# Optimization experiments

Hardware: AMD Instinct MI355X
Metric: run time of the kernel (lower is better)

## Reference

```python
import jax, jax.numpy as jnp
import numpy as np
from jax import lax

B_, L, DM = 2, 2048, 1024
DI, N, K, R = 2048, 16, 4, 64  # d_inner, d_state, d_conv, dt_rank
EPS = 1e-5


def setup_inputs() -> dict:
    key = jax.random.key(0)
    ks = jax.random.split(key, 12)
    w = lambda k, s: (jax.random.normal(k, s, dtype=jnp.float32) * 0.02)
    inp = {
        "x": jax.random.normal(ks[0], (B_, L, DM), dtype=jnp.float32),
        "hormone_vectors": jax.random.normal(ks[1], (B_, 64), dtype=jnp.float32),
        "norm_w": jnp.ones((DM,), dtype=jnp.float32),
        "in_proj_w": w(ks[2], (DM, 2 * DI)),
        "conv_w": w(ks[3], (DI, K)),
        "conv_b": jnp.zeros((DI,), dtype=jnp.float32),
        "x_proj_w": w(ks[4], (DI, R + 2 * N)),
        "dt_proj_w": w(ks[5], (R, DI)),
        "dt_proj_b": jax.random.uniform(ks[6], (DI,), dtype=jnp.float32, minval=-4.0, maxval=-2.0),
        "A_log": jnp.log(jnp.broadcast_to(jnp.arange(1, N + 1, dtype=jnp.float32), (DI, N))),
        "D": jnp.ones((DI,), dtype=jnp.float32),
        "out_proj_w": w(ks[7], (DI, DM)),
    }
    return inp


def _rmsnorm(x, w, eps=EPS):
    var = jnp.mean(x * x, axis=-1, keepdims=True)
    return x * lax.rsqrt(var + eps) * w


def _causal_depthwise_conv(u, conv_w, conv_b):
    # u: [B,L,DI] -> causal depthwise conv along L with kernel K
    lhs = jnp.transpose(u, (0, 2, 1))  # [B,DI,L]
    lhs = jnp.pad(lhs, ((0, 0), (0, 0), (K - 1, 0)))
    rhs = conv_w[:, None, :]  # [DI,1,K]
    out = lax.conv_general_dilated(
        lhs, rhs, window_strides=(1,), padding="VALID",
        dimension_numbers=("NCH", "OIH", "NCH"), feature_group_count=DI)
    return jnp.transpose(out, (0, 2, 1)) + conv_b  # [B,L,DI]


def _mamba_mixer(h, in_proj_w, conv_w, conv_b, x_proj_w, dt_proj_w, dt_proj_b,
                 A_log, D, out_proj_w):
    xz = h @ in_proj_w                       # [B,L,2*DI]
    u, z = jnp.split(xz, 2, axis=-1)         # each [B,L,DI]
    u = jax.nn.silu(_causal_depthwise_conv(u, conv_w, conv_b))

    xdbl = u @ x_proj_w                      # [B,L,R+2N]
    dt_r = xdbl[..., :R]
    Bm = xdbl[..., R:R + N]                  # [B,L,N]
    Cm = xdbl[..., R + N:]                   # [B,L,N]
    dt = jax.nn.softplus(dt_r @ dt_proj_w + dt_proj_b)  # [B,L,DI]
    A = -jnp.exp(A_log)                      # [DI,N]

    def step(hst, inp):
        dt_t, B_t, C_t, u_t = inp            # [B,DI],[B,N],[B,N],[B,DI]
        dA = jnp.exp(dt_t[..., None] * A)                         # [B,DI,N]
        dBu = dt_t[..., None] * B_t[:, None, :] * u_t[..., None]  # [B,DI,N]
        hst = dA * hst + dBu
        y = jnp.einsum("bdn,bn->bd", hst, C_t)
        return hst, y

    xs = (jnp.swapaxes(dt, 0, 1), jnp.swapaxes(Bm, 0, 1),
          jnp.swapaxes(Cm, 0, 1), jnp.swapaxes(u, 0, 1))
    h0 = jnp.zeros((u.shape[0], DI, N), dtype=u.dtype)
    _, ys = lax.scan(step, h0, xs)
    y = jnp.swapaxes(ys, 0, 1) + u * D       # [B,L,DI]
    y = y * jax.nn.silu(z)
    return y @ out_proj_w                    # [B,L,DM]


def reference(x, hormone_vectors, norm_w, in_proj_w, conv_w, conv_b, x_proj_w,
              dt_proj_w, dt_proj_b, A_log, D, out_proj_w):
    del hormone_vectors  # unused, matching original module
    h = _rmsnorm(x, norm_w)
    return x + _mamba_mixer(h, in_proj_w, conv_w, conv_b, x_proj_w,
                            dt_proj_w, dt_proj_b, A_log, D, out_proj_w)
```

## Files before the change

### kernel.cpp

```cpp
#include <hip/hip_runtime.h>
#include <stddef.h>

#define B_SZ 2
#define L_SZ 2048
#define DM_SZ 1024
#define DI_SZ 2048
#define N_SZ 16
#define K_SZ 4
#define R_SZ 64
#define ROWS (B_SZ * L_SZ)
#define CH 32
#define NCH (L_SZ / CH)
#define PS_SLICE (B_SZ * DI_SZ * N_SZ)

typedef unsigned short u16;
typedef unsigned int u32;
typedef short bf16x8 __attribute__((ext_vector_type(8)));
typedef float f32x4 __attribute__((ext_vector_type(4)));

__device__ __forceinline__ u16 f2bf(float f) {
    union { float f; u32 i; } v; v.f = f;
    u32 x = v.i;
    return (u16)((x + 0x7FFFu + ((x >> 16) & 1u)) >> 16);
}
__device__ __forceinline__ float bf2f(u16 u) {
    union { u32 i; float f; } v; v.i = ((u32)u) << 16; return v.f;
}

__device__ __forceinline__ void gload_lds16(const void* g, void* l) {
    __builtin_amdgcn_global_load_lds((const __attribute__((address_space(1))) u32*)g,
                                     (__attribute__((address_space(3))) u32*)l, 16, 0, 0);
}

__global__ __launch_bounds__(256) void rmsnorm_kernel(const float* __restrict__ x,
                                                      const float* __restrict__ w,
                                                      u16* __restrict__ h) {
    const int row = blockIdx.x;
    const float* xr = x + (size_t)row * DM_SZ;
    const int t4 = threadIdx.x * 4;
    float4 xv = *(const float4*)(xr + t4);
    float ss = xv.x * xv.x + xv.y * xv.y + xv.z * xv.z + xv.w * xv.w;
    #pragma unroll
    for (int off = 32; off; off >>= 1) ss += __shfl_down(ss, off);
    __shared__ float red[4];
    if ((threadIdx.x & 63) == 0) red[threadIdx.x >> 6] = ss;
    __syncthreads();
    float tot = red[0] + red[1] + red[2] + red[3];
    float rs = rsqrtf(tot * (1.0f / DM_SZ) + 1e-5f);
    float4 wv = *(const float4*)(w + t4);
    ushort4 o;
    o.x = f2bf(xv.x * rs * wv.x);
    o.y = f2bf(xv.y * rs * wv.y);
    o.z = f2bf(xv.z * rs * wv.z);
    o.w = f2bf(xv.w * rs * wv.w);
    *(ushort4*)(h + (size_t)row * DM_SZ + t4) = o;
}

__global__ __launch_bounds__(256) void transpose_bf16_kernel(const float* __restrict__ W,
                                                             u16* __restrict__ Wt,
                                                             int K, int N) {
    __shared__ float t[32][33];
    const int n0 = blockIdx.x * 32, k0 = blockIdx.y * 32;
    const int tx = threadIdx.x & 31, ty = threadIdx.x >> 5;
    #pragma unroll
    for (int p = 0; p < 4; ++p)
        t[ty + p * 8][tx] = W[(size_t)(k0 + ty + p * 8) * N + n0 + tx];
    __syncthreads();
    #pragma unroll
    for (int p = 0; p < 4; ++p)
        Wt[(size_t)(n0 + ty + p * 8) * K + k0 + tx] = f2bf(t[tx][ty + p * 8]);
}

template <bool HAS_RESID>
__global__ __launch_bounds__(256, 2) void mfma_gemm_bt(const u16* __restrict__ A,
                                                       const u16* __restrict__ Bt,
                                                       float* __restrict__ C,
                                                       const float* __restrict__ resid,
                                                       int M, int N, int Kd) {
    __shared__ __align__(16) u16 As[128 * 32];
    __shared__ __align__(16) u16 Bs[128 * 32];
    const int tid = threadIdx.x;
    const int lane = tid & 63;
    const int w = tid >> 6;
    const int wm = w >> 1, wn = w & 1;
    const int bm = blockIdx.y * 128, bn = blockIdx.x * 128;

    const int r0 = (w * 2 + 0) * 16 + (lane >> 2);
    const int r1 = (w * 2 + 1) * 16 + (lane >> 2);
    const int kc = (lane & 3) * 8;
    const u16* Aq0 = A + (size_t)(bm + r0) * Kd + kc;
    const u16* Aq1 = A + (size_t)(bm + r1) * Kd + kc;
    const u16* Bq0 = Bt + (size_t)(bn + r0) * Kd + kc;
    const u16* Bq1 = Bt + (size_t)(bn + r1) * Kd + kc;
    u16* lA0 = As + (w * 2 + 0) * 512;
    u16* lA1 = As + (w * 2 + 1) * 512;
    u16* lB0 = Bs + (w * 2 + 0) * 512;
    u16* lB1 = Bs + (w * 2 + 1) * 512;

    f32x4 acc[4][4] = {};
    const int fm = (lane & 15);
    const int q8 = (lane >> 4) * 8;

    for (int k0 = 0; k0 < Kd; k0 += 32) {
        gload_lds16(Aq0 + k0, lA0);
        gload_lds16(Aq1 + k0, lA1);
        gload_lds16(Bq0 + k0, lB0);
        gload_lds16(Bq1 + k0, lB1);
        __syncthreads();
        bf16x8 af[4], bf[4];
        #pragma unroll
        for (int i = 0; i < 4; ++i)
            af[i] = *(const bf16x8*)&As[(wm * 64 + i * 16 + fm) * 32 + q8];
        #pragma unroll
        for (int j = 0; j < 4; ++j)
            bf[j] = *(const bf16x8*)&Bs[(wn * 64 + j * 16 + fm) * 32 + q8];
        #pragma unroll
        for (int i = 0; i < 4; ++i)
            #pragma unroll
            for (int j = 0; j < 4; ++j)
                acc[i][j] = __builtin_amdgcn_mfma_f32_16x16x32_bf16(af[i], bf[j], acc[i][j], 0, 0, 0);
        __syncthreads();
    }

    const int crow0 = bm + wm * 64 + (lane >> 4) * 4;
    const int ccol0 = bn + wn * 64 + (lane & 15);
    #pragma unroll
    for (int i = 0; i < 4; ++i) {
        #pragma unroll
        for (int r = 0; r < 4; ++r) {
            const int row = crow0 + i * 16 + r;
            #pragma unroll
            for (int j = 0; j < 4; ++j) {
                const int col = ccol0 + j * 16;
                float v = acc[i][j][r];
                if (HAS_RESID) v += resid[(size_t)row * N + col];
                C[(size_t)row * N + col] = v;
            }
        }
    }
}

__global__ __launch_bounds__(256) void conv_silu_kernel(const float* __restrict__ xz,
                                                        const float* __restrict__ cw,
                                                        const float* __restrict__ cb,
                                                        u16* __restrict__ u) {
    const int idx = blockIdx.x * 256 + threadIdx.x;
    const int d = idx & (DI_SZ - 1);
    const int r = idx >> 11;
    const int t = r & (L_SZ - 1);
    float4 w4 = *(const float4*)(cw + (d << 2));
    const float w[4] = {w4.x, w4.y, w4.z, w4.w};
    float acc = cb[d];
    const float* base = xz + (size_t)r * (2 * DI_SZ) + d;
    #pragma unroll
    for (int k = 0; k < 4; ++k) {
        int tt = t - 3 + k;
        if (tt >= 0) acc += base[(ptrdiff_t)(k - 3) * (2 * DI_SZ)] * w[k];
    }
    u[idx] = f2bf(acc / (1.0f + __expf(-acc)));
}

__global__ __launch_bounds__(256) void xproj_mfma(const u16* __restrict__ ubf,
                                                  const u16* __restrict__ Wt,
                                                  float* __restrict__ xdbl) {
    const int lane = threadIdx.x & 63;
    const int w = threadIdx.x >> 6;
    const int m0 = blockIdx.x * 64 + w * 16;
    const int k0 = blockIdx.y * 256;
    const int fr = lane & 15;
    const int q8 = (lane >> 4) * 8;
    const u16* Arow = ubf + (size_t)(m0 + fr) * DI_SZ + k0 + q8;
    const u16* Brow = Wt + (size_t)fr * DI_SZ + k0 + q8;
    f32x4 acc[6] = {};
    #pragma unroll 2
    for (int kk = 0; kk < 256; kk += 32) {
        bf16x8 a = *(const bf16x8*)(Arow + kk);
        #pragma unroll
        for (int j = 0; j < 6; ++j) {
            bf16x8 b = *(const bf16x8*)(Brow + (size_t)(j * 16) * DI_SZ + kk);
            acc[j] = __builtin_amdgcn_mfma_f32_16x16x32_bf16(a, b, acc[j], 0, 0, 0);
        }
    }
    const int row0 = m0 + (lane >> 4) * 4;
    const int col = lane & 15;
    #pragma unroll
    for (int j = 0; j < 6; ++j)
        #pragma unroll
        for (int r = 0; r < 4; ++r)
            atomicAdd(&xdbl[(size_t)(row0 + r) * 96 + j * 16 + col], acc[j][r]);
}

__global__ __launch_bounds__(256) void dtproj_kernel(const float* __restrict__ xdbl,
                                                     const float* __restrict__ W,
                                                     const float* __restrict__ bias,
                                                     float* __restrict__ dt) {
    const int col = blockIdx.x * 256 + threadIdx.x;
    const int row0 = blockIdx.y * 8;
    __shared__ float dr[8][64];
    for (int idx = threadIdx.x; idx < 512; idx += 256) {
        int r = idx >> 6, k = idx & 63;
        dr[r][k] = xdbl[(size_t)(row0 + r) * 96 + k];
    }
    __syncthreads();
    float acc[8] = {};
    #pragma unroll 8
    for (int k = 0; k < 64; ++k) {
        float wv = W[(size_t)k * DI_SZ + col];
        #pragma unroll
        for (int r = 0; r < 8; ++r) acc[r] += dr[r][k] * wv;
    }
    const float b = bias[col];
    #pragma unroll
    for (int r = 0; r < 8; ++r) {
        float v = acc[r] + b;
        float sp = (v > 20.0f) ? v : log1pf(__expf(v));
        dt[(size_t)(row0 + r) * DI_SZ + col] = sp;
    }
}

__global__ __launch_bounds__(64) void scan_pass1(const float* __restrict__ dt,
                                                 const u16* __restrict__ u,
                                                 const float* __restrict__ xdbl,
                                                 const float* __restrict__ A_log,
                                                 float* __restrict__ P,
                                                 float* __restrict__ S) {
    const int c     = blockIdx.x & (NCH - 1);
    const int dtile = (blockIdx.x >> 6) & 31;
    const int b     = blockIdx.x >> 11;
    const int d     = dtile * 64 + threadIdx.x;
    float A[N_SZ];
    #pragma unroll
    for (int n = 0; n < N_SZ; ++n) A[n] = -expf(A_log[d * N_SZ + n]);
    __shared__ __align__(16) float bs[CH][16];
    const size_t rbase = (size_t)b * L_SZ + c * CH;
    for (int idx = threadIdx.x; idx < CH * 16; idx += 64) {
        int tt = idx >> 4, j = idx & 15;
        bs[tt][j] = xdbl[(rbase + tt) * 96 + 64 + j];
    }
    __syncthreads();
    float h[N_SZ] = {};
    float p[N_SZ];
    #pragma unroll
    for (int n = 0; n < N_SZ; ++n) p[n] = 1.0f;
    float dtv = dt[rbase * DI_SZ + d];
    float uv  = bf2f(u[rbase * DI_SZ + d]);
    for (int ti = 0; ti < CH; ++ti) {
        float dtn = 0.0f, un = 0.0f;
        if (ti + 1 < CH) {
            dtn = dt[(rbase + ti + 1) * DI_SZ + d];
            un  = bf2f(u[(rbase + ti + 1) * DI_SZ + d]);
        }
        const float dtu = dtv * uv;
        float bv[N_SZ];
        #pragma unroll
        for (int q = 0; q < 4; ++q) *(float4*)&bv[q * 4] = *(const float4*)&bs[ti][q * 4];
        #pragma unroll
        for (int n = 0; n < N_SZ; ++n) {
            float dA = __expf(dtv * A[n]);
            p[n] *= dA;
            h[n] = dA * h[n] + dtu * bv[n];
        }
        dtv = dtn; uv = un;
    }
    const size_t base = (size_t)c * PS_SLICE + ((size_t)b * DI_SZ + d) * N_SZ;
    #pragma unroll
    for (int q = 0; q < 4; ++q) {
        *(float4*)&P[base + q * 4] = make_float4(p[q*4], p[q*4+1], p[q*4+2], p[q*4+3]);
        *(float4*)&S[base + q * 4] = make_float4(h[q*4], h[q*4+1], h[q*4+2], h[q*4+3]);
    }
}

__global__ __launch_bounds__(256) void scan_pass2(float* __restrict__ P,
                                                  float* __restrict__ S) {
    const int i = blockIdx.x * 256 + threadIdx.x;
    float h = 0.0f;
    for (int c = 0; c < NCH; ++c) {
        const size_t idx = (size_t)c * PS_SLICE + i;
        const float p = P[idx];
        const float s = S[idx];
        S[idx] = h;
        h = p * h + s;
    }
}

__global__ __launch_bounds__(64) void scan_pass3(const float* __restrict__ dt,
                                                 const u16* __restrict__ u,
                                                 const float* __restrict__ xz,
                                                 const float* __restrict__ xdbl,
                                                 const float* __restrict__ A_log,
                                                 const float* __restrict__ Dw,
                                                 const float* __restrict__ H0,
                                                 u16* __restrict__ y) {
    const int c     = blockIdx.x & (NCH - 1);
    const int dtile = (blockIdx.x >> 6) & 31;
    const int b     = blockIdx.x >> 11;
    const int d     = dtile * 64 + threadIdx.x;
    float A[N_SZ];
    #pragma unroll
    for (int n = 0; n < N_SZ; ++n) A[n] = -expf(A_log[d * N_SZ + n]);
    const float Dd = Dw[d];
    __shared__ __align__(16) float bc[CH][32];
    const size_t rbase = (size_t)b * L_SZ + c * CH;
    for (int idx = threadIdx.x; idx < CH * 32; idx += 64) {
        int tt = idx >> 5, j = idx & 31;
        bc[tt][j] = xdbl[(rbase + tt) * 96 + 64 + j];
    }
    __syncthreads();
    float h[N_SZ];
    const size_t hbase = (size_t)c * PS_SLICE + ((size_t)b * DI_SZ + d) * N_SZ;
    #pragma unroll
    for (int q = 0; q < 4; ++q) *(float4*)&h[q * 4] = *(const float4*)&H0[hbase + q * 4];
    float dtv = dt[rbase * DI_SZ + d];
    float uv  = bf2f(u[rbase * DI_SZ + d]);
    float zv  = xz[rbase * (2 * DI_SZ) + DI_SZ + d];
    for (int ti = 0; ti < CH; ++ti) {
        float dtn = 0.0f, un = 0.0f, zn = 0.0f;
        if (ti + 1 < CH) {
            const size_t rn = rbase + ti + 1;
            dtn = dt[rn * DI_SZ + d];
            un  = bf2f(u[rn * DI_SZ + d]);
            zn  = xz[rn * (2 * DI_SZ) + DI_SZ + d];
        }
        const float dtu = dtv * uv;
        float bv[32];
        #pragma unroll
        for (int q = 0; q < 8; ++q) *(float4*)&bv[q * 4] = *(const float4*)&bc[ti][q * 4];
        float yv = 0.0f;
        #pragma unroll
        for (int n = 0; n < N_SZ; ++n) {
            float dA = __expf(dtv * A[n]);
            h[n] = dA * h[n] + dtu * bv[n];
            yv += h[n] * bv[16 + n];
        }
        const float sz = zv / (1.0f + __expf(-zv));
        y[(rbase + ti) * DI_SZ + d] = f2bf((yv + uv * Dd) * sz);
        dtv = dtn; uv = un; zv = zn;
    }
}

extern "C" void kernel_launch(void* const* d_in, const int* in_sizes, int n_in,
                              void* d_out, int out_size, void* d_ws, size_t ws_size,
                              hipStream_t stream) {
    const float* x         = (const float*)d_in[0];
    const float* norm_w    = (const float*)d_in[2];
    const float* in_proj_w = (const float*)d_in[3];
    const float* conv_w    = (const float*)d_in[4];
    const float* conv_b    = (const float*)d_in[5];
    const float* x_proj_w  = (const float*)d_in[6];
    const float* dt_proj_w = (const float*)d_in[7];
    const float* dt_proj_b = (const float*)d_in[8];
    const float* A_log     = (const float*)d_in[9];
    const float* Dw        = (const float*)d_in[10];
    const float* out_proj_w= (const float*)d_in[11];
    float* out = (float*)d_out;

    char* ws = (char*)d_ws;
    size_t off = 0;
    u16* y      = (u16*)(ws + off);    off += (size_t)ROWS * DI_SZ * 2;
    u16* h      = y;
    float* xz   = (float*)(ws + off);  off += (size_t)ROWS * 2 * DI_SZ * 4;
    u16* u      = (u16*)(ws + off);    off += (size_t)ROWS * DI_SZ * 2;
    float* xdbl = (float*)(ws + off);  off += (size_t)ROWS * 96 * 4;
    float* dt   = (float*)(ws + off);  off += (size_t)ROWS * DI_SZ * 4;
    float* P    = (float*)(ws + off);  off += (size_t)NCH * PS_SLICE * 4;
    float* S    = (float*)(ws + off);  off += (size_t)NCH * PS_SLICE * 4;
    u16* ipw_t  = (u16*)(ws + off);    off += (size_t)(2 * DI_SZ) * DM_SZ * 2;
    u16* opw_t  = (u16*)(ws + off);    off += (size_t)DM_SZ * DI_SZ * 2;
    u16* xpw_t  = (u16*)(ws + off);    off += (size_t)96 * DI_SZ * 2;
    (void)ws_size; (void)out_size; (void)n_in; (void)in_sizes;

    rmsnorm_kernel<<<ROWS, 256, 0, stream>>>(x, norm_w, h);
    transpose_bf16_kernel<<<dim3(2 * DI_SZ / 32, DM_SZ / 32), 256, 0, stream>>>(
        in_proj_w, ipw_t, DM_SZ, 2 * DI_SZ);
    transpose_bf16_kernel<<<dim3(DM_SZ / 32, DI_SZ / 32), 256, 0, stream>>>(
        out_proj_w, opw_t, DI_SZ, DM_SZ);
    transpose_bf16_kernel<<<dim3(96 / 32, DI_SZ / 32), 256, 0, stream>>>(
        x_proj_w, xpw_t, DI_SZ, 96);
    mfma_gemm_bt<false><<<dim3(2 * DI_SZ / 128, ROWS / 128), 256, 0, stream>>>(
        h, ipw_t, xz, nullptr, ROWS, 2 * DI_SZ, DM_SZ);
    conv_silu_kernel<<<(ROWS * DI_SZ) / 256, 256, 0, stream>>>(xz, conv_w, conv_b, u);
    hipMemsetAsync(xdbl, 0, (size_t)ROWS * 96 * 4, stream);
    xproj_mfma<<<dim3(ROWS / 64, 8), 256, 0, stream>>>(u, xpw_t, xdbl);
    dtproj_kernel<<<dim3(DI_SZ / 256, ROWS / 8), 256, 0, stream>>>(xdbl, dt_proj_w, dt_proj_b, dt);
    scan_pass1<<<B_SZ * 32 * NCH, 64, 0, stream>>>(dt, u, xdbl, A_log, P, S);
    scan_pass2<<<PS_SLICE / 256, 256, 0, stream>>>(P, S);
    scan_pass3<<<B_SZ * 32 * NCH, 64, 0, stream>>>(dt, u, xz, xdbl, A_log, Dw, S, y);
    mfma_gemm_bt<true><<<dim3(DM_SZ / 128, ROWS / 128), 256, 0, stream>>>(
        y, opw_t, out, x, ROWS, DM_SZ, DI_SZ);
}
```

Measured before the change: 391.3 us.

## Run dt projection on bf16 MFMA and store dt as bf16

Replaces the scalar FP32 dt projection with a bf16 MFMA GEMM. It adds a kernel that slices the dt-rank columns of xdbl into bf16 and a transpose of dt_proj_w into bf16. The dt tensor is now stored as bf16, halving its footprint for both scan passes that read it. In exchange there are two extra small launches and lower precision for dt, which feeds the exponentials in the scan.

```diff
diff --git a/kernel.cpp b/kernel.cpp
--- a/kernel.cpp
+++ b/kernel.cpp
@@ -190,35 +190,73 @@
             atomicAdd(&xdbl[(size_t)(row0 + r) * 96 + j * 16 + col], acc[j][r]);
 }
 
-__global__ __launch_bounds__(256) void dtproj_kernel(const float* __restrict__ xdbl,
-                                                     const float* __restrict__ W,
-                                                     const float* __restrict__ bias,
-                                                     float* __restrict__ dt) {
-    const int col = blockIdx.x * 256 + threadIdx.x;
-    const int row0 = blockIdx.y * 8;
-    __shared__ float dr[8][64];
-    for (int idx = threadIdx.x; idx < 512; idx += 256) {
-        int r = idx >> 6, k = idx & 63;
-        dr[r][k] = xdbl[(size_t)(row0 + r) * 96 + k];
+__global__ __launch_bounds__(256) void dtslice_bf16_kernel(const float* __restrict__ xdbl,
+                                                           u16* __restrict__ out) {
+    const int idx = blockIdx.x * 256 + threadIdx.x;
+    const int r = idx >> 6, k = idx & 63;
+    out[idx] = f2bf(xdbl[(size_t)r * 96 + k]);
+}
+
+__global__ __launch_bounds__(256, 2) void dtproj_mfma(const u16* __restrict__ Axd,
+                                                      const u16* __restrict__ Wt,
+                                                      const float* __restrict__ bias,
+                                                      u16* __restrict__ dt) {
+    __shared__ __align__(16) u16 As[128 * 64];
+    __shared__ __align__(16) u16 Bs[128 * 64];
+    const int tid = threadIdx.x;
+    const int lane = tid & 63;
+    const int w = tid >> 6;
+    const int wm = w >> 1, wn = w & 1;
+    const int bm = blockIdx.y * 128, bn = blockIdx.x * 128;
+
+    #pragma unroll
+    for (int q = 0; q < 4; ++q) {
+        const int rr = (w * 4 + q) * 8 + (lane >> 3);
+        const int kc = (lane & 7) * 8;
+        gload_lds16(Axd + (size_t)(bm + rr) * 64 + kc, As + (w * 4 + q) * 512);
+        gload_lds16(Wt  + (size_t)(bn + rr) * 64 + kc, Bs + (w * 4 + q) * 512);
     }
     __syncthreads();
-    float acc[8] = {};
-    #pragma unroll 8
-    for (int k = 0; k < 64; ++k) {
-        float wv = W[(size_t)k * DI_SZ + col];
-        #pragma unroll
-        for (int r = 0; r < 8; ++r) acc[r] += dr[r][k] * wv;
-    }
-    const float b = bias[col];
-    #pragma unroll
-    for (int r = 0; r < 8; ++r) {
-        float v = acc[r] + b;
-        float sp = (v > 20.0f) ? v : log1pf(__expf(v));
-        dt[(size_t)(row0 + r) * DI_SZ + col] = sp;
-    }
-}
-
-__global__ __launch_bounds__(64) void scan_pass1(const float* __restrict__ dt,
+
+    const int fm = lane & 15;
+    const int q8 = (lane >> 4) * 8;
+    f32x4 acc[4][4] = {};
+    #pragma unroll
+    for (int k0 = 0; k0 < 64; k0 += 32) {
+        bf16x8 af[4], bf[4];
+        #pragma unroll
+        for (int i = 0; i < 4; ++i)
+            af[i] = *(const bf16x8*)&As[(wm * 64 + i * 16 + fm) * 64 + k0 + q8];
+        #pragma unroll
+        for (int j = 0; j < 4; ++j)
+            bf[j] = *(const bf16x8*)&Bs[(wn * 64 + j * 16 + fm) * 64 + k0 + q8];
+        #pragma unroll
+        for (int i = 0; i < 4; ++i)
+            #pragma unroll
+            for (int j = 0; j < 4; ++j)
+                acc[i][j] = __builtin_amdgcn_mfma_f32_16x16x32_bf16(af[i], bf[j], acc[i][j], 0, 0, 0);
+    }
+
+    const int crow0 = bm + wm * 64 + (lane >> 4) * 4;
+    const int ccol0 = bn + wn * 64 + (lane & 15);
+    #pragma unroll
+    for (int j = 0; j < 4; ++j) {
+        const int col = ccol0 + j * 16;
+        const float b = bias[col];
+        #pragma unroll
+        for (int i = 0; i < 4; ++i) {
+            #pragma unroll
+            for (int r = 0; r < 4; ++r) {
+                const int row = crow0 + i * 16 + r;
+                float v = acc[i][j][r] + b;
+                float sp = (v > 20.0f) ? v : log1pf(__expf(v));
+                dt[(size_t)row * DI_SZ + col] = f2bf(sp);
+            }
+        }
+    }
+}
+
+__global__ __launch_bounds__(64) void scan_pass1(const u16* __restrict__ dt,
                                                  const u16* __restrict__ u,
                                                  const float* __restrict__ xdbl,
                                                  const float* __restrict__ A_log,
@@ -242,12 +280,12 @@
     float p[N_SZ];
     #pragma unroll
     for (int n = 0; n < N_SZ; ++n) p[n] = 1.0f;
-    float dtv = dt[rbase * DI_SZ + d];
+    float dtv = bf2f(dt[rbase * DI_SZ + d]);
     float uv  = bf2f(u[rbase * DI_SZ + d]);
     for (int ti = 0; ti < CH; ++ti) {
         float dtn = 0.0f, un = 0.0f;
         if (ti + 1 < CH) {
-            dtn = dt[(rbase + ti + 1) * DI_SZ + d];
+            dtn = bf2f(dt[(rbase + ti + 1) * DI_SZ + d]);
             un  = bf2f(u[(rbase + ti + 1) * DI_SZ + d]);
         }
         const float dtu = dtv * uv;
@@ -283,7 +321,7 @@
     }
 }
 
-__global__ __launch_bounds__(64) void scan_pass3(const float* __restrict__ dt,
+__global__ __launch_bounds__(64) void scan_pass3(const u16* __restrict__ dt,
                                                  const u16* __restrict__ u,
                                                  const float* __restrict__ xz,
                                                  const float* __restrict__ xdbl,
@@ -310,14 +348,14 @@
     const size_t hbase = (size_t)c * PS_SLICE + ((size_t)b * DI_SZ + d) * N_SZ;
     #pragma unroll
     for (int q = 0; q < 4; ++q) *(float4*)&h[q * 4] = *(const float4*)&H0[hbase + q * 4];
-    float dtv = dt[rbase * DI_SZ + d];
+    float dtv = bf2f(dt[rbase * DI_SZ + d]);
     float uv  = bf2f(u[rbase * DI_SZ + d]);
     float zv  = xz[rbase * (2 * DI_SZ) + DI_SZ + d];
     for (int ti = 0; ti < CH; ++ti) {
         float dtn = 0.0f, un = 0.0f, zn = 0.0f;
         if (ti + 1 < CH) {
             const size_t rn = rbase + ti + 1;
-            dtn = dt[rn * DI_SZ + d];
+            dtn = bf2f(dt[rn * DI_SZ + d]);
             un  = bf2f(u[rn * DI_SZ + d]);
             zn  = xz[rn * (2 * DI_SZ) + DI_SZ + d];
         }
@@ -361,12 +399,14 @@
     float* xz   = (float*)(ws + off);  off += (size_t)ROWS * 2 * DI_SZ * 4;
     u16* u      = (u16*)(ws + off);    off += (size_t)ROWS * DI_SZ * 2;
     float* xdbl = (float*)(ws + off);  off += (size_t)ROWS * 96 * 4;
-    float* dt   = (float*)(ws + off);  off += (size_t)ROWS * DI_SZ * 4;
+    u16* dt     = (u16*)(ws + off);    off += (size_t)ROWS * DI_SZ * 2;
     float* P    = (float*)(ws + off);  off += (size_t)NCH * PS_SLICE * 4;
     float* S    = (float*)(ws + off);  off += (size_t)NCH * PS_SLICE * 4;
     u16* ipw_t  = (u16*)(ws + off);    off += (size_t)(2 * DI_SZ) * DM_SZ * 2;
     u16* opw_t  = (u16*)(ws + off);    off += (size_t)DM_SZ * DI_SZ * 2;
     u16* xpw_t  = (u16*)(ws + off);    off += (size_t)96 * DI_SZ * 2;
+    u16* dtw_t  = (u16*)(ws + off);    off += (size_t)DI_SZ * R_SZ * 2;
+    u16* xdbl_bf= (u16*)(ws + off);    off += (size_t)ROWS * R_SZ * 2;
     (void)ws_size; (void)out_size; (void)n_in; (void)in_sizes;
 
     rmsnorm_kernel<<<ROWS, 256, 0, stream>>>(x, norm_w, h);
@@ -376,12 +416,16 @@
         out_proj_w, opw_t, DI_SZ, DM_SZ);
     transpose_bf16_kernel<<<dim3(96 / 32, DI_SZ / 32), 256, 0, stream>>>(
         x_proj_w, xpw_t, DI_SZ, 96);
+    transpose_bf16_kernel<<<dim3(DI_SZ / 32, R_SZ / 32), 256, 0, stream>>>(
+        dt_proj_w, dtw_t, R_SZ, DI_SZ);
     mfma_gemm_bt<false><<<dim3(2 * DI_SZ / 128, ROWS / 128), 256, 0, stream>>>(
         h, ipw_t, xz, nullptr, ROWS, 2 * DI_SZ, DM_SZ);
     conv_silu_kernel<<<(ROWS * DI_SZ) / 256, 256, 0, stream>>>(xz, conv_w, conv_b, u);
     hipMemsetAsync(xdbl, 0, (size_t)ROWS * 96 * 4, stream);
     xproj_mfma<<<dim3(ROWS / 64, 8), 256, 0, stream>>>(u, xpw_t, xdbl);
-    dtproj_kernel<<<dim3(DI_SZ / 256, ROWS / 8), 256, 0, stream>>>(xdbl, dt_proj_w, dt_proj_b, dt);
+    dtslice_bf16_kernel<<<(ROWS * R_SZ) / 256, 256, 0, stream>>>(xdbl, xdbl_bf);
+    dtproj_mfma<<<dim3(DI_SZ / 128, ROWS / 128), 256, 0, stream>>>(
+        xdbl_bf, dtw_t, dt_proj_b, dt);
     scan_pass1<<<B_SZ * 32 * NCH, 64, 0, stream>>>(dt, u, xdbl, A_log, P, S);
     scan_pass2<<<PS_SLICE / 256, 256, 0, stream>>>(P, S);
     scan_pass3<<<B_SZ * 32 * NCH, 64, 0, stream>>>(dt, u, xz, xdbl, A_log, Dw, S, y);
```

New measurement: 375.1 us. 1.04x faster.
